# Optimization experiments

Hardware: AMD Instinct MI355X
Metric: run time of the kernel (lower is better)

## Reference

```python
import jax, jax.numpy as jnp
import numpy as np

N = 500000       # total points
V = 60000        # number of voxels (segments)
XYZ_NORM = jnp.array([20.0, 20.0, 4.0], dtype=jnp.float32)
LN_EPS = 1e-3


def _ln(x, g, b):
    m = jnp.mean(x, axis=-1, keepdims=True)
    v = jnp.var(x, axis=-1, keepdims=True)
    return (x - m) * jax.lax.rsqrt(v + LN_EPS) * g + b


def _mlp_layer(x, w, b, g, be):
    # Linear -> LayerNorm -> ReLU (build_mlp in SST)
    return jax.nn.relu(_ln(x @ w + b, g, be))


def setup_inputs() -> dict:
    key = jax.random.key(0)
    ks = jax.random.split(key, 16)
    d = {
        "points": jax.random.normal(ks[0], (N, 4), jnp.float32) * 10.0,
        "features": jax.random.normal(ks[1], (N, 125), jnp.float32),
        "coors": jax.random.randint(ks[2], (N,), 0, V, jnp.int32),
        "f_cluster": jax.random.normal(ks[3], (N, 3), jnp.float32),
        "w1": jax.random.normal(ks[4], (128, 128), jnp.float32) * 0.05,
        "b1": jnp.zeros((128,), jnp.float32),
        "g1": jnp.ones((128,), jnp.float32),
        "be1": jnp.zeros((128,), jnp.float32),
        "w2": jax.random.normal(ks[5], (128, 256), jnp.float32) * 0.05,
        "b2": jnp.zeros((256,), jnp.float32),
        "g2": jnp.ones((256,), jnp.float32),
        "be2": jnp.zeros((256,), jnp.float32),
        "pw1": jax.random.normal(ks[6], (256, 256), jnp.float32) * 0.05,
        "pb1": jnp.zeros((256,), jnp.float32),
        "pg1": jnp.ones((256,), jnp.float32),
        "pbe1": jnp.zeros((256,), jnp.float32),
        "pw2": jax.random.normal(ks[7], (256, 256), jnp.float32) * 0.05,
        "pb2": jnp.zeros((256,), jnp.float32),
        "pg2": jnp.ones((256,), jnp.float32),
        "pbe2": jnp.zeros((256,), jnp.float32),
        "ow": jax.random.normal(ks[8], (256, 64), jnp.float32) * 0.05,
        "ob": jnp.zeros((64,), jnp.float32),
        "og": jnp.ones((64,), jnp.float32),
        "obe": jnp.zeros((64,), jnp.float32),
    }
    return d


def reference(points, features, coors, f_cluster,
              w1, b1, g1, be1, w2, b2, g2, be2,
              pw1, pb1, pg1, pbe1, pw2, pb2, pg2, pbe2,
              ow, ob, og, obe):
    fc = f_cluster / XYZ_NORM[None, :]
    x = jnp.concatenate([features, fc], axis=1)           # [N, 128]
    x = _mlp_layer(x, w1, b1, g1, be1)                     # [N, 128]
    x = _mlp_layer(x, w2, b2, g2, be2)                     # [N, 256]

    out_pts_feats = _mlp_layer(x, ow, ob, og, obe)         # [N, 64]

    counts = jax.ops.segment_sum(jnp.ones((x.shape[0],), x.dtype), coors,
                                 num_segments=V)           # [V]
    occ = counts > 0

    # scatter max aggregation
    agg = jax.ops.segment_max(x, coors, num_segments=V)    # [V, 256]
    agg = jnp.where(occ[:, None], agg, 0.0)
    agg = _mlp_layer(agg, pw1, pb1, pg1, pbe1)
    agg_feats = _mlp_layer(agg, pw2, pb2, pg2, pbe2)       # [V, 256]

    # scatter avg of xyz (computed in the original, used for out_coors path)
    xyz_sum = jax.ops.segment_sum(points[:, :3], coors, num_segments=V)
    cluster_xyz = xyz_sum / jnp.maximum(counts, 1.0)[:, None]
    out_coors = jnp.arange(V, dtype=jnp.int32)             # unique voxel ids
    del cluster_xyz  # not returned by the original forward

    return (out_pts_feats, agg_feats, out_coors)
```

## Files before the change

kernel.cpp:

```cpp
#include <hip/hip_runtime.h>


typedef __attribute__((ext_vector_type(4))) float f32x4;
typedef __attribute__((ext_vector_type(8))) short s16x8;
typedef __attribute__((ext_vector_type(2))) unsigned int u32x2;
typedef __attribute__((ext_vector_type(4))) unsigned int u32x4;

static constexpr int NP = 500000;
static constexpr int NV = 60000;

__device__ __forceinline__ unsigned short f2bf(float f){
  unsigned int u = __float_as_uint(f);
  u = (u + 0x7FFFu + ((u >> 16) & 1u)) >> 16;
  return (unsigned short)u;
}

__device__ __forceinline__ unsigned int cvtpk(float lo, float hi){
  unsigned int r;
  asm("v_cvt_pk_bf16_f32 %0, %1, %2" : "=v"(r) : "v"(lo), "v"(hi));
  return r;
}

__device__ __forceinline__ unsigned int pkmaxu16(unsigned int a, unsigned int b){
  unsigned int r;
  asm("v_pk_max_u16 %0, %1, %2" : "=v"(r) : "v"(a), "v"(b));
  return r;
}

__device__ __forceinline__ void pack_one(const float* __restrict__ w,
                                         unsigned short* __restrict__ dst,
                                         int K, int C, bool perm, int idx){
  int j = idx & 7, l = (idx >> 3) & 63, rest = idx >> 9;
  int kcn = K >> 5;
  int kc = rest % kcn, n = rest / kcn;
  int g = l >> 4, t = l & 15;
  int k = perm ? (kc * 32 + ((j >> 2) << 4) + g * 4 + (j & 3))
               : (kc * 32 + g * 8 + j);
  dst[idx] = f2bf(w[(size_t)k * C + n * 16 + t]);
}

__global__ void pack_hist_kernel(const float* __restrict__ w1, const float* __restrict__ w2,
                                 const float* __restrict__ ow, const float* __restrict__ pw1,
                                 const float* __restrict__ pw2,
                                 unsigned short* __restrict__ w1p, unsigned short* __restrict__ w2p,
                                 unsigned short* __restrict__ owp, unsigned short* __restrict__ pw1p,
                                 unsigned short* __restrict__ pw2p,
                                 float* __restrict__ out_coors,
                                 const int* __restrict__ coors, int* __restrict__ counts){
  int stride = gridDim.x * blockDim.x;
  const int T = 196608 + NV + NP;
  for (int i = blockIdx.x * blockDim.x + threadIdx.x; i < T; i += stride){
    if      (i < 16384)       pack_one(w1,  w1p,  128, 128, false, i);
    else if (i < 49152)       pack_one(w2,  w2p,  128, 256, true,  i - 16384);
    else if (i < 65536)       pack_one(ow,  owp,  256, 64,  true,  i - 49152);
    else if (i < 131072)      pack_one(pw1, pw1p, 256, 256, true,  i - 65536);
    else if (i < 196608)      pack_one(pw2, pw2p, 256, 256, true,  i - 131072);
    else if (i < 196608 + NV) out_coors[i - 196608] = (float)(i - 196608);
    else                      atomicAdd(&counts[coors[i - 196608 - NV]], 1);
  }
}

__global__ __launch_bounds__(1024)
void scan_kernel(const int* __restrict__ counts, int* __restrict__ cursor){
  __shared__ int part[1024];
  const int t = threadIdx.x;
  constexpr int PER = (NV + 1023) / 1024;
  int s = 0;
  for (int i = 0; i < PER; ++i){ int v = i * 1024 + t; if (v < NV) s += counts[v]; }
  part[t] = s;
  __syncthreads();
  for (int d = 1; d < 1024; d <<= 1){
    int u = (t >= d) ? part[t - d] : 0;
    __syncthreads();
    part[t] += u;
    __syncthreads();
  }
  int run = (t > 0) ? part[t - 1] : 0;
  for (int i = 0; i < PER; ++i){
    int v = i * 1024 + t;
    if (v < NV){ cursor[v] = run; run += counts[v]; }
  }
}

__global__ void scatter_prep_kernel(const int* __restrict__ coors, int* __restrict__ cursor,
                                    const float* __restrict__ feats,
                                    const float* __restrict__ fclus,
                                    int2* __restrict__ pv,
                                    unsigned int* __restrict__ x0u){
  int stride = gridDim.x * blockDim.x;
  for (int i = blockIdx.x * blockDim.x + threadIdx.x; i < NP; i += stride){
    int v = coors[i];
    int p = atomicAdd(&cursor[v], 1);
    pv[p] = make_int2(i, v);
    const float* rp = feats + (size_t)i * 125;
    unsigned int* dst = x0u + (size_t)p * 64;
#pragma unroll
    for (int k = 0; k < 15; ++k){
      f32x4 a = *(const f32x4*)(rp + k * 8);
      f32x4 b = *(const f32x4*)(rp + k * 8 + 4);
      u32x4 o;
      o[0] = cvtpk(a[0], a[1]); o[1] = cvtpk(a[2], a[3]);
      o[2] = cvtpk(b[0], b[1]); o[3] = cvtpk(b[2], b[3]);
      *(u32x4*)(dst + k * 4) = o;
    }
    {
      f32x4 a = *(const f32x4*)(rp + 120);
      const float* fc = fclus + (size_t)i * 3;
      u32x4 o;
      o[0] = cvtpk(a[0], a[1]);
      o[1] = cvtpk(a[2], a[3]);
      o[2] = cvtpk(rp[124], fc[0] * 0.05f);
      o[3] = cvtpk(fc[1] * 0.05f, fc[2] * 0.25f);
      *(u32x4*)(dst + 60) = o;
    }
  }
}

template<int KC, int NT>
__device__ __forceinline__ void gemm2x(const s16x8* bA, const s16x8* bB,
                                       const unsigned short* __restrict__ Wp,
                                       int lane, f32x4* dA, f32x4* dB){
#pragma unroll
  for (int n = 0; n < NT; ++n){
    f32x4 aA = {0.f,0.f,0.f,0.f}, aB = {0.f,0.f,0.f,0.f};
#pragma unroll
    for (int kc = 0; kc < KC; ++kc){
      s16x8 w = *(const s16x8*)(Wp + ((n * KC + kc) * 64 + lane) * 8);
      aA = __builtin_amdgcn_mfma_f32_16x16x32_bf16(w, bA[kc], aA, 0, 0, 0);
      aB = __builtin_amdgcn_mfma_f32_16x16x32_bf16(w, bB[kc], aB, 0, 0, 0);
    }
    dA[n] = aA; dB[n] = aB;
  }
}

template<int NT, int C>
__device__ __forceinline__ void bias_ln_relu_sw(f32x4* d0, f32x4* d1,
                                                const float* __restrict__ bias,
                                                const float* __restrict__ gam,
                                                const float* __restrict__ bet, int g){
  float s0 = 0.f, s1 = 0.f, q0 = 0.f, q1 = 0.f;
#pragma unroll
  for (int n = 0; n < NT; ++n){
    f32x4 bv = *(const f32x4*)(bias + n * 16 + g * 4);
#pragma unroll
    for (int i = 0; i < 4; ++i){
      float v0 = d0[n][i] + bv[i]; d0[n][i] = v0; s0 += v0; q0 += v0 * v0;
      float v1 = d1[n][i] + bv[i]; d1[n][i] = v1; s1 += v1; q1 += v1 * v1;
    }
  }
  s0 += __shfl_xor(s0, 16); s0 += __shfl_xor(s0, 32);
  q0 += __shfl_xor(q0, 16); q0 += __shfl_xor(q0, 32);
  s1 += __shfl_xor(s1, 16); s1 += __shfl_xor(s1, 32);
  q1 += __shfl_xor(q1, 16); q1 += __shfl_xor(q1, 32);
  float m0 = s0 * (1.f / C), m1 = s1 * (1.f / C);
  float r0 = rsqrtf(q0 * (1.f / C) - m0 * m0 + 1e-3f);
  float r1 = rsqrtf(q1 * (1.f / C) - m1 * m1 + 1e-3f);
#pragma unroll
  for (int n = 0; n < NT; ++n){
    f32x4 gv  = *(const f32x4*)(gam + n * 16 + g * 4);
    f32x4 bev = *(const f32x4*)(bet + n * 16 + g * 4);
#pragma unroll
    for (int i = 0; i < 4; ++i){
      d0[n][i] = fmaxf((d0[n][i] - m0) * r0 * gv[i] + bev[i], 0.f);
      d1[n][i] = fmaxf((d1[n][i] - m1) * r1 * gv[i] + bev[i], 0.f);
    }
  }
}

template<int NT>
__device__ __forceinline__ void to_frags(const f32x4* d, s16x8* f){
#pragma unroll
  for (int kc = 0; kc < NT / 2; ++kc){
    u32x4 t;
    t[0] = cvtpk(d[2*kc][0],   d[2*kc][1]);
    t[1] = cvtpk(d[2*kc][2],   d[2*kc][3]);
    t[2] = cvtpk(d[2*kc+1][0], d[2*kc+1][1]);
    t[3] = cvtpk(d[2*kc+1][2], d[2*kc+1][3]);
    f[kc] = __builtin_bit_cast(s16x8, t);
  }
}

__device__ __forceinline__ void flush4(float* __restrict__ agg, int v, int lane,
                                       unsigned int q0, unsigned int q1, bool partial){
  float* base = agg + (size_t)v * 256 + lane * 4;
  unsigned int a0 = q0 << 16, a1 = q0 & 0xffff0000u;
  unsigned int a2 = q1 << 16, a3 = q1 & 0xffff0000u;
  if (!partial){
    f32x4 o;
    o[0] = __uint_as_float(a0); o[1] = __uint_as_float(a1);
    o[2] = __uint_as_float(a2); o[3] = __uint_as_float(a3);
    *(f32x4*)base = o;
  } else {
    unsigned int* ab = (unsigned int*)base;
    atomicMax(ab + 0, a0); atomicMax(ab + 1, a1);
    atomicMax(ab + 2, a2); atomicMax(ab + 3, a3);
  }
}

__global__ __launch_bounds__(256, 2)
void point_fused_kernel(const unsigned short* __restrict__ x0,
                        const int2* __restrict__ pv,
                        const unsigned short* __restrict__ w1p,
                        const unsigned short* __restrict__ w2p,
                        const unsigned short* __restrict__ owp,
                        const float* __restrict__ b1, const float* __restrict__ g1,
                        const float* __restrict__ be1,
                        const float* __restrict__ b2, const float* __restrict__ g2,
                        const float* __restrict__ be2,
                        const float* __restrict__ ob, const float* __restrict__ og,
                        const float* __restrict__ obe,
                        float* __restrict__ agg,
                        float* __restrict__ out_pts){
  __shared__ __align__(16) unsigned short tile[4][32 * 256];
  const int lane = threadIdx.x & 63;
  const int wave = threadIdx.x >> 6;
  const int g = lane >> 4, t = lane & 15;
  const int m0 = blockIdx.x * 128 + wave * 32;
  if (m0 >= NP) return;
  const int slotA = m0 + t, slotB = m0 + 16 + t;
  const int2 pA = pv[slotA];
  const int2 pB = pv[slotB];
  const int origA = pA.x, origB = pB.x;
  const int myv = pv[m0 + (lane & 31)].y;

  s16x8 bfA[4], bfB[4];
#pragma unroll
  for (int kc = 0; kc < 4; ++kc){
    bfA[kc] = *(const s16x8*)(x0 + (size_t)slotA * 128 + (kc * 4 + g) * 8);
    bfB[kc] = *(const s16x8*)(x0 + (size_t)slotB * 128 + (kc * 4 + g) * 8);
  }

  f32x4 d1a[8], d1b[8];
  gemm2x<4, 8>(bfA, bfB, w1p, lane, d1a, d1b);
  bias_ln_relu_sw<8, 128>(d1a, d1b, b1, g1, be1, g);
  s16x8 f2a[4], f2b[4];
  to_frags<8>(d1a, f2a); to_frags<8>(d1b, f2b);

  f32x4 d2a[16], d2b[16];
  gemm2x<4, 16>(f2a, f2b, w2p, lane, d2a, d2b);
  bias_ln_relu_sw<16, 256>(d2a, d2b, b2, g2, be2, g);
  s16x8 f3a[8], f3b[8];
  to_frags<16>(d2a, f3a); to_frags<16>(d2b, f3b);

  unsigned short* my = tile[wave];
  const int rA = t, rB = t + 16;
#pragma unroll
  for (int kc = 0; kc < 8; ++kc){
    int s = kc * 4 + g;
    int spA = (s & ~7) | ((s & 7) ^ (rA & 7));
    int spB = (s & ~7) | ((s & 7) ^ (rB & 7));
    *(s16x8*)&my[rA * 256 + spA * 8] = f3a[kc];
    *(s16x8*)&my[rB * 256 + spB * 8] = f3b[kc];
  }

  {
    f32x4 d3a[4], d3b[4];
    gemm2x<8, 4>(f3a, f3b, owp, lane, d3a, d3b);
    bias_ln_relu_sw<4, 64>(d3a, d3b, ob, og, obe, g);
#pragma unroll
    for (int n = 0; n < 4; ++n){
      *(f32x4*)(out_pts + (size_t)origA * 64 + n * 16 + g * 4) = d3a[n];
      *(f32x4*)(out_pts + (size_t)origB * 64 + n * 16 + g * 4) = d3b[n];
    }
  }

  const int vleft  = (m0 > 0) ? pv[m0 - 1].y : -1;
  const int vright = (m0 + 32 < NP) ? pv[m0 + 32].y : -1;
  const int slot = lane >> 1;
  const int half = (lane & 1) * 4;
  unsigned int q0 = 0, q1 = 0;
  int cur = __shfl(myv, 0);
  int rs = 0;
  for (int r = 0; r < 32; ++r){
    int v = __shfl(myv, r);
    if (v != cur){
      flush4(agg, cur, lane, q0, q1, rs == 0 && cur == vleft);
      q0 = 0; q1 = 0; cur = v; rs = r;
    }
    int sp = (slot & ~7) | ((slot & 7) ^ (r & 7));
    u32x2 d = *(const u32x2*)&my[r * 256 + sp * 8 + half];
    q0 = pkmaxu16(q0, d[0]);
    q1 = pkmaxu16(q1, d[1]);
  }
  flush4(agg, cur, lane, q0, q1, (rs == 0 && cur == vleft) || cur == vright);
}

__global__ __launch_bounds__(256, 2)
void vox_fused_kernel(const float* __restrict__ agg,
                      const unsigned short* __restrict__ pw1p,
                      const unsigned short* __restrict__ pw2p,
                      const float* __restrict__ pb1, const float* __restrict__ pg1,
                      const float* __restrict__ pbe1,
                      const float* __restrict__ pb2, const float* __restrict__ pg2,
                      const float* __restrict__ pbe2,
                      float* __restrict__ out_vox){
  const int lane = threadIdx.x & 63;
  const int wave = threadIdx.x >> 6;
  const int m0 = blockIdx.x * 128 + wave * 32;
  if (m0 >= NV) return;
  const int g = lane >> 4, t = lane & 15;
  const size_t mA = m0 + t, mB = m0 + 16 + t;

  s16x8 bfA[8], bfB[8];
#pragma unroll
  for (int kc = 0; kc < 8; ++kc){
    const float* pa = agg + mA * 256 + kc * 32 + g * 8;
    const float* pb = agg + mB * 256 + kc * 32 + g * 8;
    f32x4 a0 = *(const f32x4*)pa, a1 = *(const f32x4*)(pa + 4);
    f32x4 b0 = *(const f32x4*)pb, b1v = *(const f32x4*)(pb + 4);
    u32x4 ta, tb;
    ta[0] = cvtpk(a0[0], a0[1]); ta[1] = cvtpk(a0[2], a0[3]);
    ta[2] = cvtpk(a1[0], a1[1]); ta[3] = cvtpk(a1[2], a1[3]);
    tb[0] = cvtpk(b0[0], b0[1]); tb[1] = cvtpk(b0[2], b0[3]);
    tb[2] = cvtpk(b1v[0], b1v[1]); tb[3] = cvtpk(b1v[2], b1v[3]);
    bfA[kc] = __builtin_bit_cast(s16x8, ta);
    bfB[kc] = __builtin_bit_cast(s16x8, tb);
  }
  f32x4 da[16], db[16];
  gemm2x<8, 16>(bfA, bfB, pw1p, lane, da, db);
  bias_ln_relu_sw<16, 256>(da, db, pb1, pg1, pbe1, g);

  s16x8 fa[8], fb[8];
  to_frags<16>(da, fa); to_frags<16>(db, fb);

  gemm2x<8, 16>(fa, fb, pw2p, lane, da, db);
  bias_ln_relu_sw<16, 256>(da, db, pb2, pg2, pbe2, g);
#pragma unroll
  for (int n = 0; n < 16; ++n){
    *(f32x4*)(out_vox + mA * 256 + n * 16 + g * 4) = da[n];
    *(f32x4*)(out_vox + mB * 256 + n * 16 + g * 4) = db[n];
  }
}

extern "C" void kernel_launch(void* const* d_in, const int* in_sizes, int n_in,
                              void* d_out, int out_size, void* d_ws, size_t ws_size,
                              hipStream_t stream){
  const float* features  = (const float*)d_in[1];
  const int*   coors     = (const int*)  d_in[2];
  const float* f_cluster = (const float*)d_in[3];
  const float* w1  = (const float*)d_in[4];
  const float* b1  = (const float*)d_in[5];
  const float* g1  = (const float*)d_in[6];
  const float* be1 = (const float*)d_in[7];
  const float* w2  = (const float*)d_in[8];
  const float* b2  = (const float*)d_in[9];
  const float* g2  = (const float*)d_in[10];
  const float* be2 = (const float*)d_in[11];
  const float* pw1 = (const float*)d_in[12];
  const float* pb1 = (const float*)d_in[13];
  const float* pg1 = (const float*)d_in[14];
  const float* pbe1= (const float*)d_in[15];
  const float* pw2 = (const float*)d_in[16];
  const float* pb2 = (const float*)d_in[17];
  const float* pg2 = (const float*)d_in[18];
  const float* pbe2= (const float*)d_in[19];
  const float* ow  = (const float*)d_in[20];
  const float* ob  = (const float*)d_in[21];
  const float* og  = (const float*)d_in[22];
  const float* obe = (const float*)d_in[23];

  char* ws = (char*)d_ws;
  float* aggf   = (float*)(ws + 0);
  int* counts   = (int*)(ws + 61500000ull);
  int* cursor   = (int*)(ws + 61800000ull);
  int2* pv      = (int2*)(ws + 62100000ull);
  unsigned int* x0u = (unsigned int*)(ws + 66200000ull);
  unsigned short* x0 = (unsigned short*)x0u;
  unsigned short* w1p = (unsigned short*)(ws + 195000000ull);
  unsigned short* w2p = (unsigned short*)(ws + 195000000ull + 1*262144ull);
  unsigned short* owp = (unsigned short*)(ws + 195000000ull + 2*262144ull);
  unsigned short* pw1p= (unsigned short*)(ws + 195000000ull + 3*262144ull);
  unsigned short* pw2p= (unsigned short*)(ws + 195000000ull + 4*262144ull);

  float* outp      = (float*)d_out;
  float* out_pts   = outp;
  float* out_vox   = outp + 32000000;
  float* out_coors = outp + 47360000;

  hipMemsetAsync(counts, 0, (size_t)NV * sizeof(int), stream);
  hipMemsetAsync(aggf,   0, (size_t)NV * 256 * sizeof(float), stream);

  pack_hist_kernel<<<2048, 256, 0, stream>>>(w1, w2, ow, pw1, pw2,
                                             w1p, w2p, owp, pw1p, pw2p,
                                             out_coors, coors, counts);

  scan_kernel<<<1, 1024, 0, stream>>>(counts, cursor);

  scatter_prep_kernel<<<2048, 256, 0, stream>>>(coors, cursor, features, f_cluster,
                                                pv, x0u);

  point_fused_kernel<<<(NP + 127) / 128, 256, 0, stream>>>(
      x0, pv, w1p, w2p, owp,
      b1, g1, be1, b2, g2, be2, ob, og, obe, aggf, out_pts);

  vox_fused_kernel<<<(NV + 127) / 128, 256, 0, stream>>>(
      aggf, pw1p, pw2p, pb1, pg1, pbe1, pb2, pg2, pbe2, out_vox);
}
```

Before: 604.3 us.

## Convert input features to bf16 in original order within pack kernel

The fp32-to-bf16 conversion of features moves from the scatter kernel, where each thread read a whole row and wrote it to its sorted slot, into the pack/histogram kernel. There, 16 threads share each row and write it in original point order, so reads and writes coalesce. The point kernel now gathers input rows by original index through pv instead of reading sorted rows. The scatter kernel shrinks to the atomic cursor pass, in exchange for scattered 256-byte row gathers in the fused point kernel and scalar per-element feature loads.

Measured after the change: 593.7 us. About the same (-1.8%).

```diff
diff --git a/kernel.cpp b/kernel.cpp
--- a/kernel.cpp
+++ b/kernel.cpp
@@ -39,24 +39,46 @@
   dst[idx] = f2bf(w[(size_t)k * C + n * 16 + t]);
 }
 
-__global__ void pack_hist_kernel(const float* __restrict__ w1, const float* __restrict__ w2,
-                                 const float* __restrict__ ow, const float* __restrict__ pw1,
-                                 const float* __restrict__ pw2,
-                                 unsigned short* __restrict__ w1p, unsigned short* __restrict__ w2p,
-                                 unsigned short* __restrict__ owp, unsigned short* __restrict__ pw1p,
-                                 unsigned short* __restrict__ pw2p,
-                                 float* __restrict__ out_coors,
-                                 const int* __restrict__ coors, int* __restrict__ counts){
+__global__ void pack_hist_prep_kernel(const float* __restrict__ feats,
+                                      const float* __restrict__ fclus,
+                                      const int* __restrict__ coors,
+                                      unsigned short* __restrict__ x0b,
+                                      const float* __restrict__ w1, const float* __restrict__ w2,
+                                      const float* __restrict__ ow, const float* __restrict__ pw1,
+                                      const float* __restrict__ pw2,
+                                      unsigned short* __restrict__ w1p, unsigned short* __restrict__ w2p,
+                                      unsigned short* __restrict__ owp, unsigned short* __restrict__ pw1p,
+                                      unsigned short* __restrict__ pw2p,
+                                      float* __restrict__ out_coors,
+                                      int* __restrict__ counts){
   int stride = gridDim.x * blockDim.x;
-  const int T = 196608 + NV + NP;
+  constexpr int PREP = NP * 16;
+  const int T = PREP + 196608 + NV + NP;
   for (int i = blockIdx.x * blockDim.x + threadIdx.x; i < T; i += stride){
-    if      (i < 16384)       pack_one(w1,  w1p,  128, 128, false, i);
-    else if (i < 49152)       pack_one(w2,  w2p,  128, 256, true,  i - 16384);
-    else if (i < 65536)       pack_one(ow,  owp,  256, 64,  true,  i - 49152);
-    else if (i < 131072)      pack_one(pw1, pw1p, 256, 256, true,  i - 65536);
-    else if (i < 196608)      pack_one(pw2, pw2p, 256, 256, true,  i - 131072);
-    else if (i < 196608 + NV) out_coors[i - 196608] = (float)(i - 196608);
-    else                      atomicAdd(&counts[coors[i - 196608 - NV]], 1);
+    if (i < PREP){
+      int r = i >> 4, cb = i & 15;
+      const float* frow = feats + (size_t)r * 125;
+      float v[8];
+#pragma unroll
+      for (int j = 0; j < 8; ++j){
+        int c = cb * 8 + j;
+        v[j] = (c < 125) ? frow[c]
+                         : fclus[(size_t)r * 3 + (c - 125)] * ((c == 127) ? 0.25f : 0.05f);
+      }
+      u32x4 o;
+      o[0] = cvtpk(v[0], v[1]); o[1] = cvtpk(v[2], v[3]);
+      o[2] = cvtpk(v[4], v[5]); o[3] = cvtpk(v[6], v[7]);
+      *(u32x4*)(x0b + (size_t)r * 128 + cb * 8) = o;
+    } else {
+      int q = i - PREP;
+      if      (q < 16384)       pack_one(w1,  w1p,  128, 128, false, q);
+      else if (q < 49152)       pack_one(w2,  w2p,  128, 256, true,  q - 16384);
+      else if (q < 65536)       pack_one(ow,  owp,  256, 64,  true,  q - 49152);
+      else if (q < 131072)      pack_one(pw1, pw1p, 256, 256, true,  q - 65536);
+      else if (q < 196608)      pack_one(pw2, pw2p, 256, 256, true,  q - 131072);
+      else if (q < 196608 + NV) out_coors[q - 196608] = (float)(q - 196608);
+      else                      atomicAdd(&counts[coors[q - 196608 - NV]], 1);
+    }
   }
 }
 
@@ -82,37 +104,13 @@
   }
 }
 
-__global__ void scatter_prep_kernel(const int* __restrict__ coors, int* __restrict__ cursor,
-                                    const float* __restrict__ feats,
-                                    const float* __restrict__ fclus,
-                                    int2* __restrict__ pv,
-                                    unsigned int* __restrict__ x0u){
+__global__ void scatter_kernel(const int* __restrict__ coors, int* __restrict__ cursor,
+                               int2* __restrict__ pv){
   int stride = gridDim.x * blockDim.x;
   for (int i = blockIdx.x * blockDim.x + threadIdx.x; i < NP; i += stride){
     int v = coors[i];
     int p = atomicAdd(&cursor[v], 1);
     pv[p] = make_int2(i, v);
-    const float* rp = feats + (size_t)i * 125;
-    unsigned int* dst = x0u + (size_t)p * 64;
-#pragma unroll
-    for (int k = 0; k < 15; ++k){
-      f32x4 a = *(const f32x4*)(rp + k * 8);
-      f32x4 b = *(const f32x4*)(rp + k * 8 + 4);
-      u32x4 o;
-      o[0] = cvtpk(a[0], a[1]); o[1] = cvtpk(a[2], a[3]);
-      o[2] = cvtpk(b[0], b[1]); o[3] = cvtpk(b[2], b[3]);
-      *(u32x4*)(dst + k * 4) = o;
-    }
-    {
-      f32x4 a = *(const f32x4*)(rp + 120);
-      const float* fc = fclus + (size_t)i * 3;
-      u32x4 o;
-      o[0] = cvtpk(a[0], a[1]);
-      o[1] = cvtpk(a[2], a[3]);
-      o[2] = cvtpk(rp[124], fc[0] * 0.05f);
-      o[3] = cvtpk(fc[1] * 0.05f, fc[2] * 0.25f);
-      *(u32x4*)(dst + 60) = o;
-    }
   }
 }
 
@@ -198,7 +196,7 @@
 }
 
 __global__ __launch_bounds__(256, 2)
-void point_fused_kernel(const unsigned short* __restrict__ x0,
+void point_fused_kernel(const unsigned short* __restrict__ x0b,
                         const int2* __restrict__ pv,
                         const unsigned short* __restrict__ w1p,
                         const unsigned short* __restrict__ w2p,
@@ -226,8 +224,8 @@
   s16x8 bfA[4], bfB[4];
 #pragma unroll
   for (int kc = 0; kc < 4; ++kc){
-    bfA[kc] = *(const s16x8*)(x0 + (size_t)slotA * 128 + (kc * 4 + g) * 8);
-    bfB[kc] = *(const s16x8*)(x0 + (size_t)slotB * 128 + (kc * 4 + g) * 8);
+    bfA[kc] = *(const s16x8*)(x0b + (size_t)origA * 128 + (kc * 4 + g) * 8);
+    bfB[kc] = *(const s16x8*)(x0b + (size_t)origB * 128 + (kc * 4 + g) * 8);
   }
 
   f32x4 d1a[8], d1b[8];
@@ -364,8 +362,7 @@
   int* counts   = (int*)(ws + 61500000ull);
   int* cursor   = (int*)(ws + 61800000ull);
   int2* pv      = (int2*)(ws + 62100000ull);
-  unsigned int* x0u = (unsigned int*)(ws + 66200000ull);
-  unsigned short* x0 = (unsigned short*)x0u;
+  unsigned short* x0b = (unsigned short*)(ws + 66200000ull);
   unsigned short* w1p = (unsigned short*)(ws + 195000000ull);
   unsigned short* w2p = (unsigned short*)(ws + 195000000ull + 1*262144ull);
   unsigned short* owp = (unsigned short*)(ws + 195000000ull + 2*262144ull);
@@ -380,17 +377,16 @@
   hipMemsetAsync(counts, 0, (size_t)NV * sizeof(int), stream);
   hipMemsetAsync(aggf,   0, (size_t)NV * 256 * sizeof(float), stream);
 
-  pack_hist_kernel<<<2048, 256, 0, stream>>>(w1, w2, ow, pw1, pw2,
-                                             w1p, w2p, owp, pw1p, pw2p,
-                                             out_coors, coors, counts);
+  pack_hist_prep_kernel<<<2048, 256, 0, stream>>>(features, f_cluster, coors, x0b,
+                                                  w1, w2, ow, pw1, pw2,
+                                                  w1p, w2p, owp, pw1p, pw2p,
+                                                  out_coors, counts);
 
   scan_kernel<<<1, 1024, 0, stream>>>(counts, cursor);
-
-  scatter_prep_kernel<<<2048, 256, 0, stream>>>(coors, cursor, features, f_cluster,
-                                                pv, x0u);
+  scatter_kernel<<<2048, 256, 0, stream>>>(coors, cursor, pv);
 
   point_fused_kernel<<<(NP + 127) / 128, 256, 0, stream>>>(
-      x0, pv, w1p, w2p, owp,
+      x0b, pv, w1p, w2p, owp,
       b1, g1, be1, b2, g2, be2, ob, og, obe, aggf, out_pts);
 
   vox_fused_kernel<<<(NV + 127) / 128, 256, 0, stream>>>(
```
